# Performance work log

Hardware: AMD Instinct MI355X
Metric: run time of the kernel (lower is better)

## Reference

```python
import jax, jax.numpy as jnp
import numpy as np


def xnorm(x, g):
    # x * gamma / ||x||_2 along last dim (no eps, matching torch.norm)
    n = jnp.sqrt(jnp.sum(x * x, axis=-1, keepdims=True))
    return x * g / n


def setup_inputs() -> dict:
    key = jax.random.key(0)
    ks = jax.random.split(key, 6)
    B, N, D = 8, 8192, 512
    H, DK, DV = 8, 64, 64
    std = 0.001
    return {
        "queries": jax.random.normal(ks[0], (B, N, D), dtype=jnp.float32),
        # weights stored [in, out] (transposed vs torch Linear)
        "Wq": jax.random.normal(ks[1], (D, H * DK), dtype=jnp.float32) * std,
        "bq": jnp.zeros((H * DK,), dtype=jnp.float32),
        "Wk": jax.random.normal(ks[2], (D, H * DK), dtype=jnp.float32) * std,
        "bk": jnp.zeros((H * DK,), dtype=jnp.float32),
        "Wv": jax.random.normal(ks[3], (D, H * DV), dtype=jnp.float32) * std,
        "bv": jnp.zeros((H * DV,), dtype=jnp.float32),
        "Wo": jax.random.normal(ks[4], (H * DV, D), dtype=jnp.float32) * std,
        "bo": jnp.zeros((D,), dtype=jnp.float32),
        "gamma": jax.random.normal(ks[5], (1, H, 1, 1), dtype=jnp.float32),
    }


def reference(queries, Wq, bq, Wk, bk, Wv, bv, Wo, bo, gamma):
    B, N, D = queries.shape
    H, DK = 8, 64
    DV = 64
    q = (queries @ Wq + bq).reshape(B, N, H, DK)  # bnhd
    k = (queries @ Wk + bk).reshape(B, N, H, DK)
    v = (queries @ Wv + bv).reshape(B, N, H, DV)
    # kv = k^T @ v per (batch, head): [B,H,DK,DV]
    kv = jnp.einsum("bnhk,bnhv->bhkv", k, v)
    kv_n = xnorm(kv, gamma)                       # norm over DV axis
    q_n = xnorm(q.transpose(0, 2, 1, 3), gamma)   # bhnd, norm over DK axis
    out = jnp.einsum("bhnk,bhkv->bnhv", q_n, kv_n).reshape(B, N, H * DV)
    return out @ Wo + bo
```

## Files before the change

### kernel.cpp

```cpp
#include <hip/hip_runtime.h>

typedef __attribute__((ext_vector_type(8))) short s8v;
typedef __attribute__((ext_vector_type(4))) short s4v;
typedef __attribute__((ext_vector_type(4))) float f4v;

__device__ __forceinline__ unsigned short f2bf(float f) {
  unsigned int u = __float_as_uint(f);
  u += 0x7FFFu + ((u >> 16) & 1u);
  return (unsigned short)(u >> 16);
}
__device__ __forceinline__ float bf2f(unsigned short s) {
  return __uint_as_float(((unsigned int)s) << 16);
}

__device__ __forceinline__ void gld16(const void* g, void* l) {
  __builtin_amdgcn_global_load_lds(
      (const __attribute__((address_space(1))) unsigned int*)g,
      (__attribute__((address_space(3))) unsigned int*)l, 16, 0, 0);
}

__global__ __launch_bounds__(256)
void convert_x_kernel(const float* __restrict__ X, unsigned short* __restrict__ Xbf)
{
  size_t base = ((size_t)blockIdx.x * 256 + threadIdx.x) * 8;
  float4 a = *(const float4*)&X[base];
  float4 b = *(const float4*)&X[base + 4];
  s8v p = (s8v){ (short)f2bf(a.x), (short)f2bf(a.y), (short)f2bf(a.z), (short)f2bf(a.w),
                 (short)f2bf(b.x), (short)f2bf(b.y), (short)f2bf(b.z), (short)f2bf(b.w) };
  *(s8v*)&Xbf[base] = p;
}

__global__ __launch_bounds__(256)
void transpose_w_kernel(const float* __restrict__ Wq, const float* __restrict__ Wk,
                        const float* __restrict__ Wv, unsigned short* __restrict__ Wt)
{
  __shared__ float T[64][68];
  const int kt = blockIdx.x, nt = blockIdx.y;
  const float* W = (nt < 8) ? Wq : (nt < 16 ? Wk : Wv);
  const int n0 = (nt & 7) * 64, k0 = kt * 64;
  const int t = threadIdx.x;
  #pragma unroll
  for (int it = 0; it < 4; ++it) {
    int idx = it * 256 + t;
    int k = idx >> 4, n4 = (idx & 15) << 2;
    *(float4*)&T[k][n4] = *(const float4*)&W[(size_t)(k0 + k) * 512 + n0 + n4];
  }
  __syncthreads();
  #pragma unroll
  for (int it = 0; it < 2; ++it) {
    int idx = it * 256 + t;
    int n = idx >> 3, k8 = (idx & 7) << 3;
    s8v p;
    #pragma unroll
    for (int j = 0; j < 8; ++j) p[j] = (short)f2bf(T[k8 + j][n]);
    *(s8v*)&Wt[((size_t)nt * 64 + n) * 512 + k0 + k8] = p;
  }
}

__global__ __launch_bounds__(256, 2)
void gemm_qkv_kernel(const unsigned short* __restrict__ Xbf,
                     const unsigned short* __restrict__ Wt,
                     const float* __restrict__ bq, const float* __restrict__ bk,
                     const float* __restrict__ bv,
                     const float* __restrict__ gamma,
                     unsigned short* __restrict__ qkv)
{
  __shared__ short As[8192];
  __shared__ short Bs[8192];
  const int t = threadIdx.x;
  const int nb = blockIdx.x, rb = blockIdx.y;
  const int wave = t >> 6, lane = t & 63;
  const int wm = wave & 1, wn = wave >> 1;
  const int quad = lane >> 4, l16 = lane & 15;
  const int row0 = rb * 128;
  const int ncol0 = nb * 128;

  const unsigned short* ap[4];
  const unsigned short* bp[4];
  #pragma unroll
  for (int i = 0; i < 4; ++i) {
    int s = i * 256 + t;
    int m = s >> 3;
    int kb = (s & 7) ^ (m & 7);
    ap[i] = Xbf + (size_t)(row0 + m) * 512 + kb * 8;
    bp[i] = Wt + (size_t)(ncol0 + m) * 512 + kb * 8;
  }

  f4v acc[4][4];
  #pragma unroll
  for (int i = 0; i < 4; ++i)
    #pragma unroll
    for (int j = 0; j < 4; ++j) acc[i][j] = (f4v){0.f, 0.f, 0.f, 0.f};

  for (int kt = 0; kt < 512; kt += 64) {
    __syncthreads();
    #pragma unroll
    for (int i = 0; i < 4; ++i) {
      int s8 = (i * 256 + t) * 8;
      gld16(ap[i] + kt, &As[s8]);
      gld16(bp[i] + kt, &Bs[s8]);
    }
    __syncthreads();
    #pragma unroll
    for (int ks = 0; ks < 2; ++ks) {
      s8v a[4], b[4];
      #pragma unroll
      for (int mi = 0; mi < 4; ++mi) {
        int r = wm * 64 + mi * 16 + l16;
        int slot = r * 8 + ((ks * 4 + quad) ^ (r & 7));
        a[mi] = *(const s8v*)&As[slot * 8];
      }
      #pragma unroll
      for (int nj = 0; nj < 4; ++nj) {
        int r = wn * 64 + nj * 16 + l16;
        int slot = r * 8 + ((ks * 4 + quad) ^ (r & 7));
        b[nj] = *(const s8v*)&Bs[slot * 8];
      }
      #pragma unroll
      for (int mi = 0; mi < 4; ++mi)
        #pragma unroll
        for (int nj = 0; nj < 4; ++nj)
          acc[mi][nj] = __builtin_amdgcn_mfma_f32_16x16x32_bf16(a[mi], b[nj], acc[mi][nj], 0, 0, 0);
    }
  }

  #pragma unroll
  for (int nj = 0; nj < 4; ++nj) {
    int colg = ncol0 + wn * 64 + nj * 16 + l16;
    float bias;
    if (colg < 512) bias = bq[colg];
    else if (colg < 1024) bias = bk[colg - 512];
    else bias = bv[colg - 1024];
    #pragma unroll
    for (int mi = 0; mi < 4; ++mi) {
      acc[mi][nj][0] += bias; acc[mi][nj][1] += bias;
      acc[mi][nj][2] += bias; acc[mi][nj][3] += bias;
    }
  }

  if (nb < 4) {
    float g = gamma[nb * 2 + wn];
    #pragma unroll
    for (int mi = 0; mi < 4; ++mi)
      #pragma unroll
      for (int rr = 0; rr < 4; ++rr) {
        float ss = acc[mi][0][rr] * acc[mi][0][rr] + acc[mi][1][rr] * acc[mi][1][rr]
                 + acc[mi][2][rr] * acc[mi][2][rr] + acc[mi][3][rr] * acc[mi][3][rr];
        ss += __shfl_xor(ss, 1);
        ss += __shfl_xor(ss, 2);
        ss += __shfl_xor(ss, 4);
        ss += __shfl_xor(ss, 8);
        float scale = g * rsqrtf(ss);
        acc[mi][0][rr] *= scale; acc[mi][1][rr] *= scale;
        acc[mi][2][rr] *= scale; acc[mi][3][rr] *= scale;
      }
  }

  const int colbase = ncol0 + wn * 64;
  #pragma unroll
  for (int mi = 0; mi < 4; ++mi)
    #pragma unroll
    for (int nj = 0; nj < 4; ++nj)
      #pragma unroll
      for (int rr = 0; rr < 4; ++rr) {
        int row = row0 + wm * 64 + mi * 16 + quad * 4 + rr;
        int col = colbase + nj * 16 + l16;
        qkv[(size_t)row * 1536 + col] = f2bf(acc[mi][nj][rr]);
      }
}

__global__ __launch_bounds__(256)
void kv_accum_kernel(const unsigned short* __restrict__ qkv, float* __restrict__ kvpart)
{
  __shared__ float ksf[16][64];
  __shared__ float vsf[16][64];
  const int t = threadIdx.x;
  const int bh = blockIdx.x, chunk = blockIdx.y;
  const int b = bh >> 3, h = bh & 7;
  const int base_row = b * 8192 + chunk * 512;
  const int lane = t & 63, wave = t >> 6;
  const int dk0 = (lane & 7) * 8, dv0 = (lane >> 3) * 8;
  const int half = t >> 7, tt = t & 127;
  const int sr = tt >> 3, u = tt & 7;
  const int col = (half ? 1024 : 512) + h * 64 + u * 8;
  const unsigned short* src = qkv + (size_t)(base_row + sr) * 1536 + col;
  float* dstlds = half ? &vsf[sr][u * 8] : &ksf[sr][u * 8];
  float acc[8][8] = {};

  for (int it = 0; it < 32; ++it) {
    __syncthreads();
    union { int4 v; unsigned short s[8]; } raw;
    raw.v = *(const int4*)(src + (size_t)it * 16 * 1536);
    float4 lo = { bf2f(raw.s[0]), bf2f(raw.s[1]), bf2f(raw.s[2]), bf2f(raw.s[3]) };
    float4 hi = { bf2f(raw.s[4]), bf2f(raw.s[5]), bf2f(raw.s[6]), bf2f(raw.s[7]) };
    *(float4*)dstlds = lo;
    *(float4*)(dstlds + 4) = hi;
    __syncthreads();
    #pragma unroll
    for (int rr = 0; rr < 4; ++rr) {
      int r = rr * 4 + wave;
      float4 ka = *(const float4*)&ksf[r][dk0];
      float4 kb = *(const float4*)&ksf[r][dk0 + 4];
      float4 va = *(const float4*)&vsf[r][dv0];
      float4 vb = *(const float4*)&vsf[r][dv0 + 4];
      float kf[8] = { ka.x, ka.y, ka.z, ka.w, kb.x, kb.y, kb.z, kb.w };
      float vf[8] = { va.x, va.y, va.z, va.w, vb.x, vb.y, vb.z, vb.w };
      #pragma unroll
      for (int i = 0; i < 8; ++i)
        #pragma unroll
        for (int j = 0; j < 8; ++j)
          acc[i][j] = fmaf(kf[i], vf[j], acc[i][j]);
    }
  }
  float* dst = kvpart + ((size_t)(chunk * 4 + wave) * 64 + bh) * 4096;
  #pragma unroll
  for (int i = 0; i < 8; ++i) {
    *(float4*)&dst[(dk0 + i) * 64 + dv0]     = (float4){ acc[i][0], acc[i][1], acc[i][2], acc[i][3] };
    *(float4*)&dst[(dk0 + i) * 64 + dv0 + 4] = (float4){ acc[i][4], acc[i][5], acc[i][6], acc[i][7] };
  }
}

__global__ __launch_bounds__(256)
void kv_reduce_kernel(const float* __restrict__ kvpart, float* __restrict__ kvbuf)
{
  const int bh = blockIdx.x, t = threadIdx.x;
  #pragma unroll
  for (int e = 0; e < 16; ++e) {
    int i = e * 256 + t;
    float s = 0.f;
    for (int c = 0; c < 64; ++c) s += kvpart[((size_t)c * 64 + bh) * 4096 + i];
    kvbuf[(size_t)bh * 4096 + i] = s;
  }
}

__global__ __launch_bounds__(256)
void build_w2t_kernel(const float* __restrict__ kvbuf, const float* __restrict__ Wo,
                      const float* __restrict__ gamma, unsigned short* __restrict__ W2t)
{
  __shared__ float WoS[512][16];
  const int b = blockIdx.x, dt = blockIdx.y;
  const int d0 = dt * 16;
  const int t = threadIdx.x;
  for (int i = 0; i < 32; ++i) {
    int flat = i * 256 + t;
    int rr_ = flat >> 4, c = flat & 15;
    WoS[rr_][c] = Wo[(size_t)rr_ * 512 + d0 + c];
  }
  __syncthreads();
  for (int rr = 0; rr < 2; ++rr) {
    int r = rr * 256 + t;
    int h = r >> 6, k = r & 63;
    const float* krow = kvbuf + ((size_t)b * 8 + h) * 4096 + (size_t)k * 64;
    float ss = 0.f;
    #pragma unroll
    for (int v = 0; v < 64; v += 4) {
      float4 x = *(const float4*)&krow[v];
      ss += x.x * x.x + x.y * x.y + x.z * x.z + x.w * x.w;
    }
    float scale = gamma[h] * rsqrtf(ss);
    f4v accv[4];
    #pragma unroll
    for (int j = 0; j < 4; ++j) accv[j] = (f4v){0.f, 0.f, 0.f, 0.f};
    for (int v = 0; v < 64; ++v) {
      float m = krow[v] * scale;
      const float* w = &WoS[h * 64 + v][0];
      #pragma unroll
      for (int j4 = 0; j4 < 4; ++j4) {
        float4 ww = *(const float4*)&w[j4 * 4];
        accv[j4][0] = fmaf(m, ww.x, accv[j4][0]);
        accv[j4][1] = fmaf(m, ww.y, accv[j4][1]);
        accv[j4][2] = fmaf(m, ww.z, accv[j4][2]);
        accv[j4][3] = fmaf(m, ww.w, accv[j4][3]);
      }
    }
    #pragma unroll
    for (int j = 0; j < 16; ++j)
      W2t[((size_t)b * 512 + d0 + j) * 512 + r] = f2bf(accv[j >> 2][j & 3]);
  }
}

__global__ __launch_bounds__(256, 2)
void gemm_out_kernel(const unsigned short* __restrict__ qkv,
                     const unsigned short* __restrict__ W2t,
                     const float* __restrict__ bo,
                     float* __restrict__ out)
{
  __shared__ short As[8192];
  __shared__ short Bs[8192];
  const int t = threadIdx.x;
  const int nb = blockIdx.x, rb = blockIdx.y;
  const int wave = t >> 6, lane = t & 63;
  const int wm = wave & 1, wn = wave >> 1;
  const int quad = lane >> 4, l16 = lane & 15;
  const int row0 = rb * 128;
  const int ncol0 = nb * 128;
  const unsigned short* Wb = W2t + (size_t)(rb >> 6) * 262144;

  const unsigned short* ap[4];
  const unsigned short* bp[4];
  #pragma unroll
  for (int i = 0; i < 4; ++i) {
    int s = i * 256 + t;
    int m = s >> 3;
    int kb = (s & 7) ^ (m & 7);
    ap[i] = qkv + (size_t)(row0 + m) * 1536 + kb * 8;
    bp[i] = Wb + (size_t)(ncol0 + m) * 512 + kb * 8;
  }

  f4v acc[4][4];
  #pragma unroll
  for (int i = 0; i < 4; ++i)
    #pragma unroll
    for (int j = 0; j < 4; ++j) acc[i][j] = (f4v){0.f, 0.f, 0.f, 0.f};

  for (int kt = 0; kt < 512; kt += 64) {
    __syncthreads();
    #pragma unroll
    for (int i = 0; i < 4; ++i) {
      int s8 = (i * 256 + t) * 8;
      gld16(ap[i] + kt, &As[s8]);
      gld16(bp[i] + kt, &Bs[s8]);
    }
    __syncthreads();
    #pragma unroll
    for (int ks = 0; ks < 2; ++ks) {
      s8v a[4], b[4];
      #pragma unroll
      for (int mi = 0; mi < 4; ++mi) {
        int r = wm * 64 + mi * 16 + l16;
        int slot = r * 8 + ((ks * 4 + quad) ^ (r & 7));
        a[mi] = *(const s8v*)&As[slot * 8];
      }
      #pragma unroll
      for (int nj = 0; nj < 4; ++nj) {
        int r = wn * 64 + nj * 16 + l16;
        int slot = r * 8 + ((ks * 4 + quad) ^ (r & 7));
        b[nj] = *(const s8v*)&Bs[slot * 8];
      }
      #pragma unroll
      for (int mi = 0; mi < 4; ++mi)
        #pragma unroll
        for (int nj = 0; nj < 4; ++nj)
          acc[mi][nj] = __builtin_amdgcn_mfma_f32_16x16x32_bf16(a[mi], b[nj], acc[mi][nj], 0, 0, 0);
    }
  }

  const int colbase = ncol0 + wn * 64;
  #pragma unroll
  for (int nj = 0; nj < 4; ++nj) {
    float bias = bo[colbase + nj * 16 + l16];
    #pragma unroll
    for (int mi = 0; mi < 4; ++mi)
      #pragma unroll
      for (int rr = 0; rr < 4; ++rr) {
        int row = row0 + wm * 64 + mi * 16 + quad * 4 + rr;
        int col = colbase + nj * 16 + l16;
        out[(size_t)row * 512 + col] = acc[mi][nj][rr] + bias;
      }
  }
}

extern "C" void kernel_launch(void* const* d_in, const int* in_sizes, int n_in,
                              void* d_out, int out_size, void* d_ws, size_t ws_size,
                              hipStream_t stream)
{
  (void)in_sizes; (void)n_in; (void)out_size; (void)ws_size;
  const float* X     = (const float*)d_in[0];
  const float* Wq    = (const float*)d_in[1];
  const float* bq    = (const float*)d_in[2];
  const float* Wk    = (const float*)d_in[3];
  const float* bk    = (const float*)d_in[4];
  const float* Wv    = (const float*)d_in[5];
  const float* bv    = (const float*)d_in[6];
  const float* Wo    = (const float*)d_in[7];
  const float* bo    = (const float*)d_in[8];
  const float* gamma = (const float*)d_in[9];

  char* ws = (char*)d_ws;
  unsigned short* qkv = (unsigned short*)ws;
  unsigned short* Xbf = (unsigned short*)(ws + 201326592);
  float* kvpart = (float*)(ws + 201326592);
  unsigned short* Wt  = (unsigned short*)(ws + 201326592 + 67108864);
  float* kvbuf        = (float*)(ws + 201326592 + 67108864 + 1572864);
  unsigned short* W2t = (unsigned short*)(ws + 201326592 + 67108864 + 1572864 + 1048576);

  dim3 blk(256);
  convert_x_kernel<<<16384, blk, 0, stream>>>(X, Xbf);
  transpose_w_kernel<<<dim3(8, 24), blk, 0, stream>>>(Wq, Wk, Wv, Wt);
  gemm_qkv_kernel<<<dim3(12, 512), blk, 0, stream>>>(Xbf, Wt, bq, bk, bv, gamma, qkv);
  kv_accum_kernel<<<dim3(64, 16), blk, 0, stream>>>(qkv, kvpart);
  kv_reduce_kernel<<<64, blk, 0, stream>>>(kvpart, kvbuf);
  build_w2t_kernel<<<dim3(8, 32), blk, 0, stream>>>(kvbuf, Wo, gamma, W2t);
  gemm_out_kernel<<<dim3(4, 512), blk, 0, stream>>>(qkv, W2t, bo, (float*)d_out);
}
```

Baseline: 577.1 us.

## Double-buffer LDS tiles in both GEMMs, swizzle block order, split kv reduce

Both bf16 GEMMs now keep two LDS buffers and issue the global-to-LDS loads for the next K tile before the MFMAs on the current tile. This replaces two barriers per iteration with one combined waitcnt+barrier, so load latency can overlap compute. Block indices are remapped through a swizzle meant to improve L2 locality across XCDs. The kv_reduce kernel is also split over 8 segments per head to expose more parallelism. The cost is doubled LDS (64KB per block), which may limit occupancy under launch_bounds(256,2).

```diff
diff --git a/kernel.cpp b/kernel.cpp
--- a/kernel.cpp
+++ b/kernel.cpp
@@ -18,6 +18,8 @@
       (const __attribute__((address_space(1))) unsigned int*)g,
       (__attribute__((address_space(3))) unsigned int*)l, 16, 0, 0);
 }
+
+#define TILE_SYNC() asm volatile("s_waitcnt vmcnt(0) lgkmcnt(0)\n\ts_barrier" ::: "memory")
 
 __global__ __launch_bounds__(256)
 void convert_x_kernel(const float* __restrict__ X, unsigned short* __restrict__ Xbf)
@@ -65,10 +67,12 @@
                      const float* __restrict__ gamma,
                      unsigned short* __restrict__ qkv)
 {
-  __shared__ short As[8192];
-  __shared__ short Bs[8192];
+  __shared__ short As[2][8192];
+  __shared__ short Bs[2][8192];
   const int t = threadIdx.x;
-  const int nb = blockIdx.x, rb = blockIdx.y;
+  const int o = blockIdx.x;
+  const int swz = (o & 7) * 768 + (o >> 3);
+  const int nb = swz % 12, rb = swz / 12;
   const int wave = t >> 6, lane = t & 63;
   const int wm = wave & 1, wn = wave >> 1;
   const int quad = lane >> 4, l16 = lane & 15;
@@ -77,6 +81,7 @@
 
   const unsigned short* ap[4];
   const unsigned short* bp[4];
+  int ldst[4];
   #pragma unroll
   for (int i = 0; i < 4; ++i) {
     int s = i * 256 + t;
@@ -84,6 +89,7 @@
     int kb = (s & 7) ^ (m & 7);
     ap[i] = Xbf + (size_t)(row0 + m) * 512 + kb * 8;
     bp[i] = Wt + (size_t)(ncol0 + m) * 512 + kb * 8;
+    ldst[i] = s * 8;
   }
 
   f4v acc[4][4];
@@ -92,15 +98,23 @@
     #pragma unroll
     for (int j = 0; j < 4; ++j) acc[i][j] = (f4v){0.f, 0.f, 0.f, 0.f};
 
-  for (int kt = 0; kt < 512; kt += 64) {
-    __syncthreads();
-    #pragma unroll
-    for (int i = 0; i < 4; ++i) {
-      int s8 = (i * 256 + t) * 8;
-      gld16(ap[i] + kt, &As[s8]);
-      gld16(bp[i] + kt, &Bs[s8]);
-    }
-    __syncthreads();
+  #pragma unroll
+  for (int i = 0; i < 4; ++i) {
+    gld16(ap[i], &As[0][ldst[i]]);
+    gld16(bp[i], &Bs[0][ldst[i]]);
+  }
+  TILE_SYNC();
+
+  for (int kt = 0; kt < 8; ++kt) {
+    const int cur = kt & 1;
+    if (kt < 7) {
+      const int koff = (kt + 1) * 64;
+      #pragma unroll
+      for (int i = 0; i < 4; ++i) {
+        gld16(ap[i] + koff, &As[cur ^ 1][ldst[i]]);
+        gld16(bp[i] + koff, &Bs[cur ^ 1][ldst[i]]);
+      }
+    }
     #pragma unroll
     for (int ks = 0; ks < 2; ++ks) {
       s8v a[4], b[4];
@@ -108,13 +122,13 @@
       for (int mi = 0; mi < 4; ++mi) {
         int r = wm * 64 + mi * 16 + l16;
         int slot = r * 8 + ((ks * 4 + quad) ^ (r & 7));
-        a[mi] = *(const s8v*)&As[slot * 8];
+        a[mi] = *(const s8v*)&As[cur][slot * 8];
       }
       #pragma unroll
       for (int nj = 0; nj < 4; ++nj) {
         int r = wn * 64 + nj * 16 + l16;
         int slot = r * 8 + ((ks * 4 + quad) ^ (r & 7));
-        b[nj] = *(const s8v*)&Bs[slot * 8];
+        b[nj] = *(const s8v*)&Bs[cur][slot * 8];
       }
       #pragma unroll
       for (int mi = 0; mi < 4; ++mi)
@@ -122,6 +136,7 @@
         for (int nj = 0; nj < 4; ++nj)
           acc[mi][nj] = __builtin_amdgcn_mfma_f32_16x16x32_bf16(a[mi], b[nj], acc[mi][nj], 0, 0, 0);
     }
+    TILE_SYNC();
   }
 
   #pragma unroll
@@ -223,10 +238,10 @@
 __global__ __launch_bounds__(256)
 void kv_reduce_kernel(const float* __restrict__ kvpart, float* __restrict__ kvbuf)
 {
-  const int bh = blockIdx.x, t = threadIdx.x;
-  #pragma unroll
-  for (int e = 0; e < 16; ++e) {
-    int i = e * 256 + t;
+  const int bh = blockIdx.x, seg = blockIdx.y, t = threadIdx.x;
+  #pragma unroll
+  for (int e = 0; e < 2; ++e) {
+    int i = seg * 512 + e * 256 + t;
     float s = 0.f;
     for (int c = 0; c < 64; ++c) s += kvpart[((size_t)c * 64 + bh) * 4096 + i];
     kvbuf[(size_t)bh * 4096 + i] = s;
@@ -285,10 +300,12 @@
                      const float* __restrict__ bo,
                      float* __restrict__ out)
 {
-  __shared__ short As[8192];
-  __shared__ short Bs[8192];
+  __shared__ short As[2][8192];
+  __shared__ short Bs[2][8192];
   const int t = threadIdx.x;
-  const int nb = blockIdx.x, rb = blockIdx.y;
+  const int o = blockIdx.x;
+  const int swz = (o & 7) * 256 + (o >> 3);
+  const int nb = swz & 3, rb = swz >> 2;
   const int wave = t >> 6, lane = t & 63;
   const int wm = wave & 1, wn = wave >> 1;
   const int quad = lane >> 4, l16 = lane & 15;
@@ -298,6 +315,7 @@
 
   const unsigned short* ap[4];
   const unsigned short* bp[4];
+  int ldst[4];
   #pragma unroll
   for (int i = 0; i < 4; ++i) {
     int s = i * 256 + t;
@@ -305,6 +323,7 @@
     int kb = (s & 7) ^ (m & 7);
     ap[i] = qkv + (size_t)(row0 + m) * 1536 + kb * 8;
     bp[i] = Wb + (size_t)(ncol0 + m) * 512 + kb * 8;
+    ldst[i] = s * 8;
   }
 
   f4v acc[4][4];
@@ -313,15 +332,23 @@
     #pragma unroll
     for (int j = 0; j < 4; ++j) acc[i][j] = (f4v){0.f, 0.f, 0.f, 0.f};
 
-  for (int kt = 0; kt < 512; kt += 64) {
-    __syncthreads();
-    #pragma unroll
-    for (int i = 0; i < 4; ++i) {
-      int s8 = (i * 256 + t) * 8;
-      gld16(ap[i] + kt, &As[s8]);
-      gld16(bp[i] + kt, &Bs[s8]);
-    }
-    __syncthreads();
+  #pragma unroll
+  for (int i = 0; i < 4; ++i) {
+    gld16(ap[i], &As[0][ldst[i]]);
+    gld16(bp[i], &Bs[0][ldst[i]]);
+  }
+  TILE_SYNC();
+
+  for (int kt = 0; kt < 8; ++kt) {
+    const int cur = kt & 1;
+    if (kt < 7) {
+      const int koff = (kt + 1) * 64;
+      #pragma unroll
+      for (int i = 0; i < 4; ++i) {
+        gld16(ap[i] + koff, &As[cur ^ 1][ldst[i]]);
+        gld16(bp[i] + koff, &Bs[cur ^ 1][ldst[i]]);
+      }
+    }
     #pragma unroll
     for (int ks = 0; ks < 2; ++ks) {
       s8v a[4], b[4];
@@ -329,13 +356,13 @@
       for (int mi = 0; mi < 4; ++mi) {
         int r = wm * 64 + mi * 16 + l16;
         int slot = r * 8 + ((ks * 4 + quad) ^ (r & 7));
-        a[mi] = *(const s8v*)&As[slot * 8];
+        a[mi] = *(const s8v*)&As[cur][slot * 8];
       }
       #pragma unroll
       for (int nj = 0; nj < 4; ++nj) {
         int r = wn * 64 + nj * 16 + l16;
         int slot = r * 8 + ((ks * 4 + quad) ^ (r & 7));
-        b[nj] = *(const s8v*)&Bs[slot * 8];
+        b[nj] = *(const s8v*)&Bs[cur][slot * 8];
       }
       #pragma unroll
       for (int mi = 0; mi < 4; ++mi)
@@ -343,6 +370,7 @@
         for (int nj = 0; nj < 4; ++nj)
           acc[mi][nj] = __builtin_amdgcn_mfma_f32_16x16x32_bf16(a[mi], b[nj], acc[mi][nj], 0, 0, 0);
     }
+    TILE_SYNC();
   }
 
   const int colbase = ncol0 + wn * 64;
@@ -387,9 +415,9 @@
   dim3 blk(256);
   convert_x_kernel<<<16384, blk, 0, stream>>>(X, Xbf);
   transpose_w_kernel<<<dim3(8, 24), blk, 0, stream>>>(Wq, Wk, Wv, Wt);
-  gemm_qkv_kernel<<<dim3(12, 512), blk, 0, stream>>>(Xbf, Wt, bq, bk, bv, gamma, qkv);
+  gemm_qkv_kernel<<<6144, blk, 0, stream>>>(Xbf, Wt, bq, bk, bv, gamma, qkv);
   kv_accum_kernel<<<dim3(64, 16), blk, 0, stream>>>(qkv, kvpart);
-  kv_reduce_kernel<<<64, blk, 0, stream>>>(kvpart, kvbuf);
+  kv_reduce_kernel<<<dim3(64, 8), blk, 0, stream>>>(kvpart, kvbuf);
   build_w2t_kernel<<<dim3(8, 32), blk, 0, stream>>>(kvbuf, Wo, gamma, W2t);
-  gemm_out_kernel<<<dim3(4, 512), blk, 0, stream>>>(qkv, W2t, bo, (float*)d_out);
-}
+  gemm_out_kernel<<<2048, blk, 0, stream>>>(qkv, W2t, bo, (float*)d_out);
+}
```

After: 551.9 us. 4.4% less time.
